# Kernel optimization log

Hardware: AMD Instinct MI355X
Metric: run time of the kernel (lower is better)

Reference implementation:

```python
import jax, jax.numpy as jnp
import numpy as np

TOP_K = 2


def setup_inputs() -> dict:
    key = jax.random.key(0)
    ks = jax.random.split(key, 7)
    B, S, H = 2, 2048, 2048
    E, A, NS = 8, 64, 16384
    x = jax.random.normal(ks[0], (B, S, H), jnp.float32)
    gate_w = jax.random.normal(ks[1], (E, H), jnp.float32) * 0.01  # nn.init std=0.01
    W = jax.random.normal(ks[2], (H, H), jnp.float32) * 0.02       # base FFN weight [out,in]
    atoms = jax.random.normal(ks[3], (A, NS), jnp.float32) * 0.02
    expert_atom_weights = jax.random.normal(ks[4], (E, A), jnp.float32) * 0.1
    importance = jax.random.normal(ks[5], (E, NS), jnp.float32) * 0.1
    mask_idx = jax.random.randint(ks[6], (NS,), 0, H * H, jnp.int32)  # flat positions in W
    return dict(x=x, gate_w=gate_w, W=W, atoms=atoms,
                expert_atom_weights=expert_atom_weights,
                importance=importance, mask_idx=mask_idx)


def reference(x, gate_w, W, atoms, expert_atom_weights, importance, mask_idx):
    B, S, H = x.shape
    xt = x.reshape(-1, H)                       # [T, H] tokens
    # --- SRDERouter ---
    logits = jnp.clip(xt @ gate_w.T, -50.0, 50.0)          # [T, E]
    top_w, top_idx = jax.lax.top_k(logits, TOP_K)          # [T, K]
    rw = jax.nn.softmax(top_w, axis=-1)                    # [T, K]
    # --- SharedDeltaVocabulary + SparseExpert importance ---
    deltas = jax.nn.softmax(expert_atom_weights, axis=-1) @ atoms   # [E, NS]
    weighted = deltas * jax.nn.sigmoid(importance)                  # [E, NS]
    # --- LearnedMaskSelector: flat idx -> (row, col) of W [out, in] ---
    rows = mask_idx // H                                   # output coords [NS]
    cols = mask_idx % H                                    # input coords  [NS]
    # per-token combined sparse delta values over selected positions
    vals = jnp.einsum('tk,tks->ts', rw, weighted[top_idx])  # [T, NS]
    xg = xt[:, cols]                                        # [T, NS] gather of inputs
    # scatter-add products into output rows: y[t, r] += sum_{j: rows[j]=r} xg[t,j]*vals[t,j]
    contrib = jax.ops.segment_sum((xg * vals).T, rows, num_segments=H)  # [H, T]
    out = xt @ W.T + contrib.T                              # base FFN + sparse expert delta
    return out.reshape(B, S, H)
```

## Files before the change

kernel.cpp:

```cpp
#include <hip/hip_runtime.h>
#include <hip/hip_bf16.h>
#include <stdint.h>

#define H       2048
#define LOGH    11
#define T_TOK   4096
#define NEXP    8
#define NATOM   64
#define NS      16384

typedef short bf16x8 __attribute__((ext_vector_type(8)));
typedef float f32x4  __attribute__((ext_vector_type(4)));

__device__ __forceinline__ unsigned short f2bf(float f) {
  union { float f; unsigned u; } c;
  c.f = f;
  c.u += 0x7fff + ((c.u >> 16) & 1);
  return (unsigned short)(c.u >> 16);
}

__global__ __launch_bounds__(256) void prep_kernel(
    const float* __restrict__ x, const float* __restrict__ gate_w,
    const float* __restrict__ W, unsigned short* __restrict__ xb,
    unsigned short* __restrict__ wb, float4* __restrict__ tokInfo) {
  const int b = blockIdx.x;
  if (b >= T_TOK / 4) {
    const int wblk = b - T_TOK / 4;
    const float4* src = reinterpret_cast<const float4*>(W);
#pragma unroll
    for (int p = 0; p < 8; ++p) {
      const int i = (wblk + p * 512) * 256 + threadIdx.x;
      float4 v = src[i];
      ushort4 o;
      o.x = f2bf(v.x); o.y = f2bf(v.y); o.z = f2bf(v.z); o.w = f2bf(v.w);
      *reinterpret_cast<ushort4*>(wb + (size_t)i * 4) = o;
    }
    return;
  }
  const int wv = threadIdx.x >> 6;
  const int lane = threadIdx.x & 63;
  const int t = b * 4 + wv;
  const float4* xr = reinterpret_cast<const float4*>(x + (size_t)t * H);
  unsigned short* xbr = xb + (size_t)t * H;

  float accs[NEXP];
#pragma unroll
  for (int e = 0; e < NEXP; ++e) accs[e] = 0.f;
#pragma unroll
  for (int it = 0; it < 8; ++it) {
    const int j4 = it * 64 + lane;
    float4 xv = xr[j4];
    ushort4 o;
    o.x = f2bf(xv.x); o.y = f2bf(xv.y); o.z = f2bf(xv.z); o.w = f2bf(xv.w);
    *reinterpret_cast<ushort4*>(xbr + (size_t)j4 * 4) = o;
#pragma unroll
    for (int e = 0; e < NEXP; ++e) {
      float4 gv = reinterpret_cast<const float4*>(gate_w + (size_t)e * H)[j4];
      accs[e] = fmaf(xv.x, gv.x, accs[e]);
      accs[e] = fmaf(xv.y, gv.y, accs[e]);
      accs[e] = fmaf(xv.z, gv.z, accs[e]);
      accs[e] = fmaf(xv.w, gv.w, accs[e]);
    }
  }
#pragma unroll
  for (int e = 0; e < NEXP; ++e) {
    float v = accs[e];
#pragma unroll
    for (int off = 32; off > 0; off >>= 1) v += __shfl_down(v, off);
    accs[e] = v;
  }
  if (lane == 0) {
    float lg[NEXP];
#pragma unroll
    for (int e = 0; e < NEXP; ++e) lg[e] = fminf(fmaxf(accs[e], -50.f), 50.f);
    int e0 = 0; float w0 = lg[0];
#pragma unroll
    for (int e = 1; e < NEXP; ++e) { if (lg[e] > w0) { w0 = lg[e]; e0 = e; } }
    int e1 = -1; float w1 = -3.4e38f;
#pragma unroll
    for (int e = 0; e < NEXP; ++e) {
      if (e == e0) continue;
      if (lg[e] > w1) { w1 = lg[e]; e1 = e; }
    }
    const float r1 = expf(w1 - w0);
    float4 ti;
    ti.x = 1.f / (1.f + r1);
    ti.y = r1 / (1.f + r1);
    ti.z = __int_as_float(e0);
    ti.w = __int_as_float(e1);
    tokInfo[t] = ti;
  }
}

__global__ __launch_bounds__(256) void weighted_kernel(
    const float* __restrict__ eaw, const float* __restrict__ atoms,
    const float* __restrict__ importance, float* __restrict__ weighted) {
  __shared__ float p[NATOM];
  const int e = blockIdx.x >> 3;
  const int chunk = blockIdx.x & 7;
  const int tid = threadIdx.x;
  if (tid < NATOM) p[tid] = eaw[e * NATOM + tid];
  __syncthreads();
  if (tid == 0) {
    float m = p[0];
    for (int a = 1; a < NATOM; ++a) m = fmaxf(m, p[a]);
    float s = 0.f;
    for (int a = 0; a < NATOM; ++a) { p[a] = expf(p[a] - m); s += p[a]; }
    float inv = 1.f / s;
    for (int a = 0; a < NATOM; ++a) p[a] *= inv;
  }
  __syncthreads();
  const int base = chunk * 2048 + tid;
  for (int it = 0; it < 8; ++it) {
    int s = base + it * 256;
    float acc = 0.f;
#pragma unroll 16
    for (int a = 0; a < NATOM; ++a) acc = fmaf(p[a], atoms[a * NS + s], acc);
    float imp = importance[e * NS + s];
    float sig = 1.f / (1.f + expf(-imp));
    weighted[e * NS + s] = acc * sig;
  }
}

__device__ __forceinline__ int sortedFlat(int pos) {
  const int l = pos >> 7, k = pos & 127;
  return ((k >> 2) << 9) | (l << 2) | (k & 3);
}

__global__ __launch_bounds__(1024) void build_sort_kernel(
    const int* __restrict__ mask_idx, int* __restrict__ elemT,
    int* __restrict__ sidSorted) {
  __shared__ int hist[H];
  __shared__ int base[H];
  __shared__ int wsum[16];
  __shared__ int wexc[16];
  const int tid = threadIdx.x;
  hist[tid] = 0;
  hist[tid + 1024] = 0;
  __syncthreads();
  for (int s = tid; s < NS; s += 1024) {
    int r = mask_idx[s] >> LOGH;
    atomicAdd(&hist[r], 1);
  }
  __syncthreads();
  int a = hist[2 * tid], b = hist[2 * tid + 1];
  int ps = a + b;
  const int lane = tid & 63, wid = tid >> 6;
#pragma unroll
  for (int off = 1; off < 64; off <<= 1) {
    int n = __shfl_up(ps, off);
    if (lane >= off) ps += n;
  }
  if (lane == 63) wsum[wid] = ps;
  __syncthreads();
  if (tid == 0) {
    int run = 0;
    for (int w = 0; w < 16; ++w) { wexc[w] = run; run += wsum[w]; }
  }
  __syncthreads();
  int ex = wexc[wid] + ps - (a + b);
  base[2 * tid] = ex;
  base[2 * tid + 1] = ex + a;
  __syncthreads();
  for (int s = tid; s < NS; s += 1024) {
    int m = mask_idx[s];
    int r = m >> LOGH, c = m & (H - 1);
    int pos = atomicAdd(&base[r], 1);
    elemT[sortedFlat(pos)] = (r << LOGH) | c;
    sidSorted[pos] = s;
  }
}

__global__ __launch_bounds__(256) void permute_weighted_kernel(
    const float* __restrict__ weighted, const int* __restrict__ sidSorted,
    float* __restrict__ wSortedT) {
  const int i = blockIdx.x * 256 + threadIdx.x;
  const int e = blockIdx.y;
  const int s = sidSorted[i];
  wSortedT[(size_t)e * NS + sortedFlat(i)] = weighted[(size_t)e * NS + s];
}

__global__ __launch_bounds__(256) void gemm_kernel(
    const unsigned short* __restrict__ xb, const unsigned short* __restrict__ wb,
    float* __restrict__ out) {
  __shared__ __align__(16) unsigned short aLds[128 * 32];
  __shared__ __align__(16) unsigned short bLds[128 * 32];
  const int tid  = threadIdx.x;
  const int wave = tid >> 6;
  const int lane = tid & 63;
  const int bid = blockIdx.x;
  const int xcd = bid & 7;
  const int j   = bid >> 3;
  const int n_t = (xcd << 1) | (j & 1);
  const int m_t = j >> 1;
  const int m0 = m_t * 128;
  const int n0 = n_t * 128;
  const int wr = wave >> 1;
  const int wc = wave & 1;

  f32x4 acc[4][4];
#pragma unroll
  for (int i = 0; i < 4; ++i)
#pragma unroll
    for (int jj = 0; jj < 4; ++jj)
#pragma unroll
      for (int r = 0; r < 4; ++r) acc[i][jj][r] = 0.f;

  const int srow = lane >> 2;
  const int kcol = (lane & 3) * 8;

  for (int k0 = 0; k0 < H; k0 += 32) {
#pragma unroll
    for (int p = 0; p < 2; ++p) {
      const int g = p * 4 + wave;
      const unsigned short* ga = xb + (size_t)(m0 + g * 16 + srow) * H + k0 + kcol;
      const unsigned short* gb = wb + (size_t)(n0 + g * 16 + srow) * H + k0 + kcol;
      __builtin_amdgcn_global_load_lds(
          (const __attribute__((address_space(1))) unsigned int*)ga,
          (__attribute__((address_space(3))) unsigned int*)(aLds + g * 16 * 32), 16, 0, 0);
      __builtin_amdgcn_global_load_lds(
          (const __attribute__((address_space(1))) unsigned int*)gb,
          (__attribute__((address_space(3))) unsigned int*)(bLds + g * 16 * 32), 16, 0, 0);
    }
    __syncthreads();

    const int kc = (lane >> 4) * 8;
    const int ar = wr * 64 + (lane & 15);
    const int br = wc * 64 + (lane & 15);
    bf16x8 af[4], bfr[4];
#pragma unroll
    for (int i = 0; i < 4; ++i)
      af[i] = *reinterpret_cast<const bf16x8*>(aLds + (ar + i * 16) * 32 + kc);
#pragma unroll
    for (int jj = 0; jj < 4; ++jj)
      bfr[jj] = *reinterpret_cast<const bf16x8*>(bLds + (br + jj * 16) * 32 + kc);
#pragma unroll
    for (int i = 0; i < 4; ++i)
#pragma unroll
      for (int jj = 0; jj < 4; ++jj)
        acc[i][jj] = __builtin_amdgcn_mfma_f32_16x16x32_bf16(af[i], bfr[jj], acc[i][jj], 0, 0, 0);
    __syncthreads();
  }

  const int cr = (lane >> 4) * 4;
  const int cc = lane & 15;
#pragma unroll
  for (int i = 0; i < 4; ++i)
#pragma unroll
    for (int jj = 0; jj < 4; ++jj)
#pragma unroll
      for (int r = 0; r < 4; ++r)
        out[(size_t)(m0 + wr * 64 + i * 16 + cr + r) * H + (n0 + wc * 64 + jj * 16 + cc)] =
            acc[i][jj][r];
}

__global__ __launch_bounds__(512) void scatter_kernel(
    const float* __restrict__ x, const float* __restrict__ wSortedT,
    const int* __restrict__ elemT, const float4* __restrict__ tokInfo,
    float* __restrict__ out) {
  __shared__ float xrow[4][H];
  __shared__ float acc[4][H];
  const int tid  = threadIdx.x;
  const int tk   = tid >> 7;
  const int l    = tid & 127;
  const int t0   = blockIdx.x * 4;

  {
    const float4* xsrc = reinterpret_cast<const float4*>(x + (size_t)t0 * H);
    float4* xdst = reinterpret_cast<float4*>(&xrow[0][0]);
    float4* adst = reinterpret_cast<float4*>(&acc[0][0]);
    float4 z; z.x = z.y = z.z = z.w = 0.f;
#pragma unroll
    for (int i = 0; i < 4; ++i) {
      xdst[tid + i * 512] = xsrc[tid + i * 512];
      adst[tid + i * 512] = z;
    }
  }
  __syncthreads();

  const int t = t0 + tk;
  const float4 ti = tokInfo[t];
  const float rw0 = ti.x, rw1 = ti.y;
  const int e0 = __float_as_int(ti.z);
  const int e1 = __float_as_int(ti.w);

  const int4*   ev4 = reinterpret_cast<const int4*>(elemT);
  const float4* w04 = reinterpret_cast<const float4*>(wSortedT + (size_t)e0 * NS);
  const float4* w14 = reinterpret_cast<const float4*>(wSortedT + (size_t)e1 * NS);
  float* xw = &xrow[tk][0];
  float* aw = &acc[tk][0];

  float accv = 0.f;
  int curR = -1;
  int flushed = 0;

  int4   ev = ev4[l];
  float4 a  = w04[l];
  float4 b  = w14[l];

#define PROC1(EV, AV, BV, GV)                                     \
  {                                                               \
    const int r = (EV) >> LOGH;                                   \
    const float ct = (GV) * fmaf(rw0, (AV), rw1 * (BV));          \
    if (r != curR) {                                              \
      if (curR >= 0) {                                            \
        if (flushed) aw[curR] = accv;                             \
        else { atomicAdd(&aw[curR], accv); flushed = 1; }         \
      }                                                           \
      curR = r; accv = ct;                                        \
    } else {                                                      \
      accv += ct;                                                 \
    }                                                             \
  }

#pragma unroll 4
  for (int s = 0; s < 32; ++s) {
    const int sn = (s + 1 <= 31) ? s + 1 : 31;
    int4   evN = ev4[sn * 128 + l];
    float4 aN  = w04[sn * 128 + l];
    float4 bN  = w14[sn * 128 + l];
    const float g0 = xw[ev.x & (H - 1)];
    const float g1 = xw[ev.y & (H - 1)];
    const float g2 = xw[ev.z & (H - 1)];
    const float g3 = xw[ev.w & (H - 1)];
    PROC1(ev.x, a.x, b.x, g0)
    PROC1(ev.y, a.y, b.y, g1)
    PROC1(ev.z, a.z, b.z, g2)
    PROC1(ev.w, a.w, b.w, g3)
    ev = evN; a = aN; b = bN;
  }
  atomicAdd(&aw[curR], accv);
  __syncthreads();
#undef PROC1

  {
    float4* orow = reinterpret_cast<float4*>(out + (size_t)t * H);
    const float4* arow = reinterpret_cast<const float4*>(aw);
#pragma unroll
    for (int i = 0; i < 4; ++i) {
      int idx = l + i * 128;
      float4 o = orow[idx];
      float4 av = arow[idx];
      o.x += av.x; o.y += av.y; o.z += av.z; o.w += av.w;
      orow[idx] = o;
    }
  }
}

extern "C" void kernel_launch(void* const* d_in, const int* in_sizes, int n_in,
                              void* d_out, int out_size, void* d_ws, size_t ws_size,
                              hipStream_t stream) {
  const float* x          = (const float*)d_in[0];
  const float* gate_w     = (const float*)d_in[1];
  const float* W          = (const float*)d_in[2];
  const float* atoms      = (const float*)d_in[3];
  const float* eaw        = (const float*)d_in[4];
  const float* importance = (const float*)d_in[5];
  const int*   mask_idx   = (const int*)d_in[6];
  float* out = (float*)d_out;

  char* ws = (char*)d_ws;
  size_t off = 0;
  unsigned short* xb = (unsigned short*)(ws + off); off += (size_t)T_TOK * H * 2;
  unsigned short* wb = (unsigned short*)(ws + off); off += (size_t)H * H * 2;
  float* weighted    = (float*)(ws + off);          off += (size_t)NEXP * NS * 4;
  float4* tokInfo    = (float4*)(ws + off);         off += (size_t)T_TOK * 16;
  int* elemT         = (int*)(ws + off);            off += (size_t)NS * 4;
  int* sidSorted     = (int*)(ws + off);            off += (size_t)NS * 4;
  float* wSortedT    = (float*)(ws + off);          off += (size_t)NEXP * NS * 4;

  prep_kernel<<<T_TOK / 4 + 512, 256, 0, stream>>>(x, gate_w, W, xb, wb, tokInfo);
  weighted_kernel<<<64, 256, 0, stream>>>(eaw, atoms, importance, weighted);
  build_sort_kernel<<<1, 1024, 0, stream>>>(mask_idx, elemT, sidSorted);
  permute_weighted_kernel<<<dim3(NS / 256, NEXP), 256, 0, stream>>>(weighted, sidSorted, wSortedT);
  gemm_kernel<<<512, 256, 0, stream>>>(xb, wb, out);
  scatter_kernel<<<T_TOK / 4, 512, 0, stream>>>(x, wSortedT, elemT, tokInfo, out);
}
```

Baseline: 285.6 us.

## Fuse delta-vocabulary computation with permutation and share atom loads across experts

Moves the per-expert atom softmax into the single-block sort kernel and rewrites weighted_kernel so each thread computes all eight experts for one slot, reading each atom column once. Results are written straight to their sorted/transposed positions through a new position map (posOfS), so the separate permute kernel and its intermediate buffer are dropped. This saves one launch and a round trip through global memory, and cuts atom reads by a factor of eight. The cost is that the weighted computation now has to wait for the serial sort kernel, and its writes land as a scattered pattern.

```diff
diff --git a/kernel.cpp b/kernel.cpp
--- a/kernel.cpp
+++ b/kernel.cpp
@@ -92,49 +92,35 @@
   }
 }
 
-__global__ __launch_bounds__(256) void weighted_kernel(
-    const float* __restrict__ eaw, const float* __restrict__ atoms,
-    const float* __restrict__ importance, float* __restrict__ weighted) {
-  __shared__ float p[NATOM];
-  const int e = blockIdx.x >> 3;
-  const int chunk = blockIdx.x & 7;
-  const int tid = threadIdx.x;
-  if (tid < NATOM) p[tid] = eaw[e * NATOM + tid];
-  __syncthreads();
-  if (tid == 0) {
-    float m = p[0];
-    for (int a = 1; a < NATOM; ++a) m = fmaxf(m, p[a]);
-    float s = 0.f;
-    for (int a = 0; a < NATOM; ++a) { p[a] = expf(p[a] - m); s += p[a]; }
-    float inv = 1.f / s;
-    for (int a = 0; a < NATOM; ++a) p[a] *= inv;
-  }
-  __syncthreads();
-  const int base = chunk * 2048 + tid;
-  for (int it = 0; it < 8; ++it) {
-    int s = base + it * 256;
-    float acc = 0.f;
-#pragma unroll 16
-    for (int a = 0; a < NATOM; ++a) acc = fmaf(p[a], atoms[a * NS + s], acc);
-    float imp = importance[e * NS + s];
-    float sig = 1.f / (1.f + expf(-imp));
-    weighted[e * NS + s] = acc * sig;
-  }
-}
-
 __device__ __forceinline__ int sortedFlat(int pos) {
   const int l = pos >> 7, k = pos & 127;
   return ((k >> 2) << 9) | (l << 2) | (k & 3);
 }
 
 __global__ __launch_bounds__(1024) void build_sort_kernel(
-    const int* __restrict__ mask_idx, int* __restrict__ elemT,
-    int* __restrict__ sidSorted) {
+    const int* __restrict__ mask_idx, const float* __restrict__ eaw,
+    int* __restrict__ elemT, int* __restrict__ posOfS, float* __restrict__ pbuf) {
   __shared__ int hist[H];
   __shared__ int base[H];
   __shared__ int wsum[16];
   __shared__ int wexc[16];
   const int tid = threadIdx.x;
+
+  if (tid < NEXP) {
+    float v[NATOM];
+#pragma unroll
+    for (int a = 0; a < NATOM; ++a) v[a] = eaw[tid * NATOM + a];
+    float m = v[0];
+#pragma unroll
+    for (int a = 1; a < NATOM; ++a) m = fmaxf(m, v[a]);
+    float ssum = 0.f;
+#pragma unroll
+    for (int a = 0; a < NATOM; ++a) { v[a] = expf(v[a] - m); ssum += v[a]; }
+    const float inv = 1.f / ssum;
+#pragma unroll
+    for (int a = 0; a < NATOM; ++a) pbuf[tid * NATOM + a] = v[a] * inv;
+  }
+
   hist[tid] = 0;
   hist[tid + 1024] = 0;
   __syncthreads();
@@ -166,18 +152,47 @@
     int m = mask_idx[s];
     int r = m >> LOGH, c = m & (H - 1);
     int pos = atomicAdd(&base[r], 1);
-    elemT[sortedFlat(pos)] = (r << LOGH) | c;
-    sidSorted[pos] = s;
-  }
-}
-
-__global__ __launch_bounds__(256) void permute_weighted_kernel(
-    const float* __restrict__ weighted, const int* __restrict__ sidSorted,
+    const int fl = sortedFlat(pos);
+    elemT[fl] = (r << LOGH) | c;
+    posOfS[s] = fl;
+  }
+}
+
+__global__ __launch_bounds__(256) void weighted_kernel(
+    const float* __restrict__ pbuf, const float* __restrict__ atoms,
+    const float* __restrict__ importance, const int* __restrict__ posOfS,
     float* __restrict__ wSortedT) {
-  const int i = blockIdx.x * 256 + threadIdx.x;
-  const int e = blockIdx.y;
-  const int s = sidSorted[i];
-  wSortedT[(size_t)e * NS + sortedFlat(i)] = weighted[(size_t)e * NS + s];
+  __shared__ float p[NEXP][NATOM];
+  const int tid = threadIdx.x;
+#pragma unroll
+  for (int i = tid; i < NEXP * NATOM; i += 256) (&p[0][0])[i] = pbuf[i];
+  __syncthreads();
+
+  const int s = blockIdx.x * 256 + tid;
+  const float* as = atoms + s;
+
+  float acc[NEXP];
+#pragma unroll
+  for (int e = 0; e < NEXP; ++e) acc[e] = 0.f;
+
+#pragma unroll
+  for (int ab = 0; ab < 8; ++ab) {
+    float v[8];
+#pragma unroll
+    for (int j = 0; j < 8; ++j) v[j] = as[(size_t)(ab * 8 + j) * NS];
+#pragma unroll
+    for (int j = 0; j < 8; ++j)
+#pragma unroll
+      for (int e = 0; e < NEXP; ++e) acc[e] = fmaf(p[e][ab * 8 + j], v[j], acc[e]);
+  }
+
+  const int fl = posOfS[s];
+#pragma unroll
+  for (int e = 0; e < NEXP; ++e) {
+    const float imp = importance[(size_t)e * NS + s];
+    const float sig = 1.f / (1.f + expf(-imp));
+    wSortedT[(size_t)e * NS + fl] = acc[e] * sig;
+  }
 }
 
 __global__ __launch_bounds__(256) void gemm_kernel(
@@ -363,16 +378,15 @@
   size_t off = 0;
   unsigned short* xb = (unsigned short*)(ws + off); off += (size_t)T_TOK * H * 2;
   unsigned short* wb = (unsigned short*)(ws + off); off += (size_t)H * H * 2;
-  float* weighted    = (float*)(ws + off);          off += (size_t)NEXP * NS * 4;
   float4* tokInfo    = (float4*)(ws + off);         off += (size_t)T_TOK * 16;
   int* elemT         = (int*)(ws + off);            off += (size_t)NS * 4;
-  int* sidSorted     = (int*)(ws + off);            off += (size_t)NS * 4;
+  int* posOfS        = (int*)(ws + off);            off += (size_t)NS * 4;
   float* wSortedT    = (float*)(ws + off);          off += (size_t)NEXP * NS * 4;
+  float* pbuf        = (float*)(ws + off);          off += (size_t)NEXP * NATOM * 4;
 
   prep_kernel<<<T_TOK / 4 + 512, 256, 0, stream>>>(x, gate_w, W, xb, wb, tokInfo);
-  weighted_kernel<<<64, 256, 0, stream>>>(eaw, atoms, importance, weighted);
-  build_sort_kernel<<<1, 1024, 0, stream>>>(mask_idx, elemT, sidSorted);
-  permute_weighted_kernel<<<dim3(NS / 256, NEXP), 256, 0, stream>>>(weighted, sidSorted, wSortedT);
+  build_sort_kernel<<<1, 1024, 0, stream>>>(mask_idx, eaw, elemT, posOfS, pbuf);
+  weighted_kernel<<<NS / 256, 256, 0, stream>>>(pbuf, atoms, importance, posOfS, wSortedT);
   gemm_kernel<<<512, 256, 0, stream>>>(xb, wb, out);
   scatter_kernel<<<T_TOK / 4, 512, 0, stream>>>(x, wSortedT, elemT, tokInfo, out);
 }
```

New measurement: 242.0 us. 1.18x faster.
